# Optimization experiments

Hardware: AMD Instinct MI355X
Metric: run time of the kernel (lower is better)

## Reference

```python
import jax, jax.numpy as jnp
import numpy as np

N = 50000   # nodes
E = 800000  # edges (avg degree 16)
F = 256     # in_feats
H = 4       # num_heads
D = 64      # out_feats per head (H*D == F)


def setup_inputs() -> dict:
    key = jax.random.key(0)
    ks = jax.random.split(key, 10)
    s = 0.02
    HD = H * D
    return {
        "feat": jax.random.normal(ks[0], (N, F), jnp.float32),
        "src": jax.random.randint(ks[1], (E,), 0, N),
        "dst": jax.random.randint(ks[2], (E,), 0, N),
        "Wq": jax.random.normal(ks[3], (HD, F), jnp.float32) * s,
        "bq": jnp.zeros((HD,), jnp.float32),
        "Wk": jax.random.normal(ks[4], (HD, F), jnp.float32) * s,
        "bk": jnp.zeros((HD,), jnp.float32),
        "Wv": jax.random.normal(ks[5], (HD, F), jnp.float32) * s,
        "bv": jnp.zeros((HD,), jnp.float32),
        "Wskip": jax.random.normal(ks[6], (HD, F), jnp.float32) * s,
        "bskip": jnp.zeros((HD,), jnp.float32),
        "Wgate": jax.random.normal(ks[7], (1, 3 * HD), jnp.float32) * s,
        "bgate": jnp.zeros((1,), jnp.float32),
        "ln_w": jnp.ones((HD,), jnp.float32),
        "ln_b": jnp.zeros((HD,), jnp.float32),
        "prelu_a": jnp.float32(0.25),
    }


def reference(feat, src, dst, Wq, bq, Wk, bk, Wv, bv, Wskip, bskip,
              Wgate, bgate, ln_w, ln_b, prelu_a):
    n = feat.shape[0]
    scale = 1.0 / np.sqrt(D).astype(np.float32)
    # projections: note DGL code names q from src nodes, k from dst nodes
    q = (feat @ Wq.T + bq).reshape(n, H, D)
    k = (feat @ Wk.T + bk).reshape(n, H, D)
    v = (feat @ Wv.T + bv).reshape(n, H, D)
    # per-edge scores: u_dot_v('ft','ft') = q[src] . k[dst], scaled
    e = jnp.einsum('ehd,ehd->eh', q[src], k[dst]) * scale  # [E, H]
    # edge softmax over incoming edges of each destination node
    m = jax.ops.segment_max(e, dst, num_segments=n)          # [N, H]
    ex = jnp.exp(e - m[dst])
    denom = jax.ops.segment_sum(ex, dst, num_segments=n)    # [N, H]
    sa = ex / denom[dst]                                     # [E, H]
    # weighted scatter-aggregate: sum_e sa * v[src]
    agg = jax.ops.segment_sum(sa[:, :, None] * v[src], dst, num_segments=n)
    rst = agg.reshape(n, H * D)
    # gated skip connection
    skip = feat @ Wskip.T + bskip
    g = jax.nn.sigmoid(
        jnp.concatenate([skip, rst, skip - rst], axis=-1) @ Wgate.T + bgate)
    rst = g * skip + (1.0 - g) * rst
    # layer norm
    mu = rst.mean(-1, keepdims=True)
    var = rst.var(-1, keepdims=True)
    rst = (rst - mu) * jax.lax.rsqrt(var + 1e-5) * ln_w + ln_b
    # PReLU
    return jnp.where(rst >= 0, rst, prelu_a * rst)
```

## Files before the change

kernel.cpp:

```cpp
#include <hip/hip_runtime.h>
#include <math.h>


typedef __attribute__((ext_vector_type(8))) short short8;
typedef __attribute__((ext_vector_type(4))) float floatx4;
typedef __attribute__((ext_vector_type(2))) float floatx2;
typedef __attribute__((address_space(3))) void lds_void;
typedef __attribute__((address_space(1))) const void gbl_void;

__device__ inline unsigned short f2bf(float x) {
    unsigned int u = __float_as_uint(x);
    u = (u + 0x7fffu + ((u >> 16) & 1u)) >> 16;
    return (unsigned short)u;
}
__device__ inline float bf2f(unsigned short u) {
    return __uint_as_float(((unsigned int)u) << 16);
}

__global__ void prep_kernel(const float* __restrict__ f, ushort* __restrict__ fb,
                            int n_elems, int total_pad,
                            const float* __restrict__ Wq, const float* __restrict__ Wk,
                            const float* __restrict__ Wv, const float* __restrict__ Wsk,
                            const float* __restrict__ bq, const float* __restrict__ bk,
                            const float* __restrict__ bv, const float* __restrict__ bsk,
                            ushort* __restrict__ Wcat, float* __restrict__ bcat,
                            int* __restrict__ counts, int* __restrict__ cursor, int n)
{
    int g = blockIdx.x * blockDim.x + threadIdx.x;
    int featQ = total_pad >> 2;
    if (g < featQ) {
        int i = g * 4;
        float4 v = (i < n_elems) ? *(const float4*)(f + i) : make_float4(0.f, 0.f, 0.f, 0.f);
        ushort4 u;
        u.x = f2bf(v.x); u.y = f2bf(v.y); u.z = f2bf(v.z); u.w = f2bf(v.w);
        *(ushort4*)(fb + i) = u;
        return;
    }
    int g2 = g - featQ;
    if (g2 < 65536) {
        int i = g2 * 4;
        int mat = i >> 16;
        int rem = i & 65535;
        const float* W = (mat == 0) ? Wq : (mat == 1) ? Wk : (mat == 2) ? Wv : Wsk;
        float4 v = *(const float4*)(W + rem);
        ushort4 u;
        u.x = f2bf(v.x); u.y = f2bf(v.y); u.z = f2bf(v.z); u.w = f2bf(v.w);
        *(ushort4*)(Wcat + i) = u;
        return;
    }
    int g3 = g2 - 65536;
    if (g3 < 256) {
        int o = g3 * 4;
        int mat = o >> 8;
        const float* b = (mat == 0) ? bq : (mat == 1) ? bk : (mat == 2) ? bv : bsk;
        *(float4*)(bcat + o) = *(const float4*)(b + (o & 255));
        return;
    }
    int g4 = g3 - 256;
    if (g4 < n) counts[g4] = 0;
    if (g4 == 0) *cursor = 0;
}


__global__ void count_kernel(const int* __restrict__ dst, int* counts, int e) {
    int i = blockIdx.x * blockDim.x + threadIdx.x;
    if (i < e) atomicAdd(&counts[dst[i]], 1);
}

__global__ void alloc_kernel(const int* __restrict__ counts, int* start, int* cur,
                             int* cursor, int n) {
    int i = blockIdx.x * blockDim.x + threadIdx.x;
    int lane = threadIdx.x & 63;
    int c = (i < n) ? counts[i] : 0;
    int incl = c;
#pragma unroll
    for (int d = 1; d < 64; d <<= 1) {
        int t = __shfl_up(incl, d);
        if (lane >= d) incl += t;
    }
    int waveTot = __shfl(incl, 63);
    int base = 0;
    if (lane == 63) base = atomicAdd(cursor, waveTot);
    base = __shfl(base, 63);
    if (i < n) {
        int s = base + incl - c;
        start[i] = s;
        cur[i] = s;
    }
}

__global__ void fill_kernel(const int* __restrict__ dst, const int* __restrict__ src,
                            int* cur, int* srclist, int e) {
    int i = blockIdx.x * blockDim.x + threadIdx.x;
    if (i < e) {
        int pos = atomicAdd(&cur[dst[i]], 1);
        srclist[pos] = src[i];
    }
}

__global__ __launch_bounds__(512) void mfma_gemm(
    const ushort* __restrict__ featb, const ushort* __restrict__ Wcat,
    const float* __restrict__ bcat,
    unsigned char* __restrict__ q8, ushort* __restrict__ kb,
    unsigned char* __restrict__ v8, ushort* __restrict__ sb, int n)
{
    __shared__ ushort At[128 * 32];
    __shared__ ushort Bt[256 * 32];
    int tid = threadIdx.x;
    int lane = tid & 63;
    int wv = tid >> 6;
    int ysel = blockIdx.x;
    int mBase = blockIdx.y * 128;
    int nBlk = ysel * 256;
    int mQuad = (wv & 1) * 64;
    int nQuad = (wv >> 1) * 64;

    floatx4 zero = {0.f, 0.f, 0.f, 0.f};
    floatx4 acc[4][4];
#pragma unroll
    for (int i = 0; i < 4; ++i)
#pragma unroll
        for (int j = 0; j < 4; ++j) acc[i][j] = zero;

    int rsel = lane & 15;
    int ksel = (lane >> 4) * 8;
    int lrow = lane >> 2;
    int lcol = (lane & 3) * 8;

    for (int k0 = 0; k0 < 256; k0 += 32) {
        {
            int row = 16 * wv + lrow;
            const ushort* gp = featb + (size_t)(mBase + row) * 256 + k0 + lcol;
            __builtin_amdgcn_global_load_lds((gbl_void*)gp, (lds_void*)&At[16 * wv * 32], 16, 0, 0);
        }
#pragma unroll
        for (int r = 0; r < 2; ++r) {
            int row = 32 * wv + 16 * r + lrow;
            const ushort* gp = Wcat + (size_t)(nBlk + row) * 256 + k0 + lcol;
            __builtin_amdgcn_global_load_lds((gbl_void*)gp, (lds_void*)&Bt[(32 * wv + 16 * r) * 32], 16, 0, 0);
        }
        __syncthreads();
        short8 af[4], bf[4];
#pragma unroll
        for (int i = 0; i < 4; ++i)
            af[i] = *(const short8*)&At[(mQuad + 16 * i + rsel) * 32 + ksel];
#pragma unroll
        for (int j = 0; j < 4; ++j)
            bf[j] = *(const short8*)&Bt[(nQuad + 16 * j + rsel) * 32 + ksel];
#pragma unroll
        for (int i = 0; i < 4; ++i)
#pragma unroll
            for (int j = 0; j < 4; ++j)
                acc[i][j] = __builtin_amdgcn_mfma_f32_16x16x32_bf16(bf[j], af[i], acc[i][j], 0, 0, 0);
        __syncthreads();
    }

    int rowq4 = (lane >> 4) * 4;
    float4 bias[4];
#pragma unroll
    for (int nt = 0; nt < 4; ++nt)
        bias[nt] = *(const float4*)(bcat + nBlk + nQuad + 16 * nt + rowq4);

    if (ysel == 0 || ysel == 2) {
        unsigned char* outp = (ysel == 0) ? q8 : v8;
#pragma unroll
        for (int mt = 0; mt < 4; ++mt) {
            int m = mBase + mQuad + 16 * mt + (lane & 15);
            if (m < n) {
                unsigned char* rowp = outp + (size_t)m * 256 + nQuad + rowq4;
#pragma unroll
                for (int nt = 0; nt < 4; ++nt) {
                    int pk = __builtin_amdgcn_cvt_pk_fp8_f32(
                        acc[mt][nt][0] + bias[nt].x, acc[mt][nt][1] + bias[nt].y, 0, false);
                    pk = __builtin_amdgcn_cvt_pk_fp8_f32(
                        acc[mt][nt][2] + bias[nt].z, acc[mt][nt][3] + bias[nt].w, pk, true);
                    *(int*)(rowp + 16 * nt) = pk;
                }
            }
        }
    } else {
        ushort* outp = (ysel == 1) ? kb : sb;
#pragma unroll
        for (int mt = 0; mt < 4; ++mt) {
            int m = mBase + mQuad + 16 * mt + (lane & 15);
            if (m < n) {
                ushort* rowp = outp + (size_t)m * 256 + nQuad + rowq4;
#pragma unroll
                for (int nt = 0; nt < 4; ++nt) {
                    uint lo = (uint)f2bf(acc[mt][nt][0] + bias[nt].x)
                            | ((uint)f2bf(acc[mt][nt][1] + bias[nt].y) << 16);
                    uint hi = (uint)f2bf(acc[mt][nt][2] + bias[nt].z)
                            | ((uint)f2bf(acc[mt][nt][3] + bias[nt].w) << 16);
                    *(uint2*)(rowp + 16 * nt) = make_uint2(lo, hi);
                }
            }
        }
    }
}

__global__ __launch_bounds__(256) void node_kernel(
    const unsigned char* __restrict__ q8, const ushort* __restrict__ kb,
    const unsigned char* __restrict__ v8, const ushort* __restrict__ sbuf,
    const int* __restrict__ srclist, const int* __restrict__ start,
    const int* __restrict__ counts,
    const float* __restrict__ Wg, const float* __restrict__ bg,
    const float* __restrict__ lnw, const float* __restrict__ lnb,
    const float* __restrict__ pa,
    float* __restrict__ out, int n, int E)
{
    int wvi = threadIdx.x >> 6;
    int lane = threadIdx.x & 63;
    int node = blockIdx.x * 4 + wvi;
    if (node >= n) return;

    int l32 = lane & 31;
    int half = lane >> 5;
    int f0 = l32 * 8;

    short8 kv = *(const short8*)(kb + (size_t)node * 256 + f0);
    float kf[8];
#pragma unroll
    for (int i = 0; i < 8; ++i) kf[i] = bf2f((unsigned short)kv[i]);

    float acc[8];
#pragma unroll
    for (int i = 0; i < 8; ++i) acc[i] = 0.f;
    float denom = 0.f;

    int sidx = start[node], cnt = counts[node];

    for (int base = 0; base < cnt; base += 64) {
        int m = min(64, cnt - base);
        int batch = srclist[min(sidx + base + lane, E - 1)];
        for (int j = 0; j < m; j += 4) {
            int j0 = j + half;
            int j1 = j0 + 2;
            bool vld0 = j0 < m;
            bool vld1 = j1 < m;
            int s0 = __shfl(batch, vld0 ? j0 : j);
            int s1 = __shfl(batch, vld1 ? j1 : j);
            uint2 qw0 = *(const uint2*)(q8 + (size_t)s0 * 256 + f0);
            uint2 vw0 = *(const uint2*)(v8 + (size_t)s0 * 256 + f0);
            uint2 qw1 = *(const uint2*)(q8 + (size_t)s1 * 256 + f0);
            uint2 vw1 = *(const uint2*)(v8 + (size_t)s1 * 256 + f0);

            floatx2 qa0 = __builtin_amdgcn_cvt_pk_f32_fp8(qw0.x, false);
            floatx2 qa1 = __builtin_amdgcn_cvt_pk_f32_fp8(qw0.x, true);
            floatx2 qa2 = __builtin_amdgcn_cvt_pk_f32_fp8(qw0.y, false);
            floatx2 qa3 = __builtin_amdgcn_cvt_pk_f32_fp8(qw0.y, true);
            floatx2 qb0 = __builtin_amdgcn_cvt_pk_f32_fp8(qw1.x, false);
            floatx2 qb1 = __builtin_amdgcn_cvt_pk_f32_fp8(qw1.x, true);
            floatx2 qb2 = __builtin_amdgcn_cvt_pk_f32_fp8(qw1.y, false);
            floatx2 qb3 = __builtin_amdgcn_cvt_pk_f32_fp8(qw1.y, true);

            float p0 = qa0[0]*kf[0] + qa0[1]*kf[1] + qa1[0]*kf[2] + qa1[1]*kf[3]
                     + qa2[0]*kf[4] + qa2[1]*kf[5] + qa3[0]*kf[6] + qa3[1]*kf[7];
            float p1 = qb0[0]*kf[0] + qb0[1]*kf[1] + qb1[0]*kf[2] + qb1[1]*kf[3]
                     + qb2[0]*kf[4] + qb2[1]*kf[5] + qb3[0]*kf[6] + qb3[1]*kf[7];
            p0 += __shfl_xor(p0, 1);  p1 += __shfl_xor(p1, 1);
            p0 += __shfl_xor(p0, 2);  p1 += __shfl_xor(p1, 2);
            p0 += __shfl_xor(p0, 4);  p1 += __shfl_xor(p1, 4);
            float w0 = vld0 ? __expf(p0 * 0.125f) : 0.f;
            float w1 = vld1 ? __expf(p1 * 0.125f) : 0.f;

            floatx2 va0 = __builtin_amdgcn_cvt_pk_f32_fp8(vw0.x, false);
            floatx2 va1 = __builtin_amdgcn_cvt_pk_f32_fp8(vw0.x, true);
            floatx2 va2 = __builtin_amdgcn_cvt_pk_f32_fp8(vw0.y, false);
            floatx2 va3 = __builtin_amdgcn_cvt_pk_f32_fp8(vw0.y, true);
            floatx2 vb0 = __builtin_amdgcn_cvt_pk_f32_fp8(vw1.x, false);
            floatx2 vb1 = __builtin_amdgcn_cvt_pk_f32_fp8(vw1.x, true);
            floatx2 vb2 = __builtin_amdgcn_cvt_pk_f32_fp8(vw1.y, false);
            floatx2 vb3 = __builtin_amdgcn_cvt_pk_f32_fp8(vw1.y, true);

            denom += w0 + w1;
            acc[0] = fmaf(w0, va0[0], fmaf(w1, vb0[0], acc[0]));
            acc[1] = fmaf(w0, va0[1], fmaf(w1, vb0[1], acc[1]));
            acc[2] = fmaf(w0, va1[0], fmaf(w1, vb1[0], acc[2]));
            acc[3] = fmaf(w0, va1[1], fmaf(w1, vb1[1], acc[3]));
            acc[4] = fmaf(w0, va2[0], fmaf(w1, vb2[0], acc[4]));
            acc[5] = fmaf(w0, va2[1], fmaf(w1, vb2[1], acc[5]));
            acc[6] = fmaf(w0, va3[0], fmaf(w1, vb3[0], acc[6]));
            acc[7] = fmaf(w0, va3[1], fmaf(w1, vb3[1], acc[7]));
        }
    }

#pragma unroll
    for (int i = 0; i < 8; ++i) acc[i] += __shfl_xor(acc[i], 32);
    denom += __shfl_xor(denom, 32);
    float inv = (denom > 0.f) ? 1.f / denom : 0.f;
    float r[8];
#pragma unroll
    for (int i = 0; i < 8; ++i) r[i] = acc[i] * inv;

    short8 sv = *(const short8*)(sbuf + (size_t)node * 256 + f0);
    float s[8];
#pragma unroll
    for (int i = 0; i < 8; ++i) s[i] = bf2f((unsigned short)sv[i]);

    float4 wa0 = *(const float4*)(Wg + f0);
    float4 wa1 = *(const float4*)(Wg + f0 + 4);
    float4 wb0 = *(const float4*)(Wg + 256 + f0);
    float4 wb1 = *(const float4*)(Wg + 256 + f0 + 4);
    float4 wc0 = *(const float4*)(Wg + 512 + f0);
    float4 wc1 = *(const float4*)(Wg + 512 + f0 + 4);
    float z = wa0.x*s[0] + wa0.y*s[1] + wa0.z*s[2] + wa0.w*s[3]
            + wa1.x*s[4] + wa1.y*s[5] + wa1.z*s[6] + wa1.w*s[7]
            + wb0.x*r[0] + wb0.y*r[1] + wb0.z*r[2] + wb0.w*r[3]
            + wb1.x*r[4] + wb1.y*r[5] + wb1.z*r[6] + wb1.w*r[7]
            + wc0.x*(s[0]-r[0]) + wc0.y*(s[1]-r[1]) + wc0.z*(s[2]-r[2]) + wc0.w*(s[3]-r[3])
            + wc1.x*(s[4]-r[4]) + wc1.y*(s[5]-r[5]) + wc1.z*(s[6]-r[6]) + wc1.w*(s[7]-r[7]);
#pragma unroll
    for (int d = 16; d >= 1; d >>= 1) z += __shfl_xor(z, d);
    z += bg[0];
    float g = 1.f / (1.f + __expf(-z));

    float y[8];
#pragma unroll
    for (int i = 0; i < 8; ++i) y[i] = g * s[i] + (1.f - g) * r[i];

    float sum = y[0]+y[1]+y[2]+y[3]+y[4]+y[5]+y[6]+y[7];
#pragma unroll
    for (int d = 16; d >= 1; d >>= 1) sum += __shfl_xor(sum, d);
    float mu = sum * (1.f / 256.f);
    float dv[8];
    float sq = 0.f;
#pragma unroll
    for (int i = 0; i < 8; ++i) { dv[i] = y[i] - mu; sq = fmaf(dv[i], dv[i], sq); }
#pragma unroll
    for (int d = 16; d >= 1; d >>= 1) sq += __shfl_xor(sq, d);
    float rstd = rsqrtf(sq * (1.f / 256.f) + 1e-5f);

    float4 lw0 = *(const float4*)(lnw + f0);
    float4 lw1 = *(const float4*)(lnw + f0 + 4);
    float4 lb0 = *(const float4*)(lnb + f0);
    float4 lb1 = *(const float4*)(lnb + f0 + 4);
    float lwv[8] = {lw0.x, lw0.y, lw0.z, lw0.w, lw1.x, lw1.y, lw1.z, lw1.w};
    float lbv[8] = {lb0.x, lb0.y, lb0.z, lb0.w, lb1.x, lb1.y, lb1.z, lb1.w};
    float ap = pa[0];
    float o[8];
#pragma unroll
    for (int i = 0; i < 8; ++i) {
        float t = dv[i] * rstd * lwv[i] + lbv[i];
        o[i] = (t >= 0.f) ? t : ap * t;
    }

    float4 stv;
    stv.x = half ? o[4] : o[0];
    stv.y = half ? o[5] : o[1];
    stv.z = half ? o[6] : o[2];
    stv.w = half ? o[7] : o[3];
    *(float4*)(out + (size_t)node * 256 + f0 + 4 * half) = stv;
}


extern "C" void kernel_launch(void* const* d_in, const int* in_sizes, int n_in,
                              void* d_out, int out_size, void* d_ws, size_t ws_size,
                              hipStream_t stream)
{
    const float* feat = (const float*)d_in[0];
    const int* src    = (const int*)d_in[1];
    const int* dst    = (const int*)d_in[2];
    const float* Wq   = (const float*)d_in[3];
    const float* bq   = (const float*)d_in[4];
    const float* Wk   = (const float*)d_in[5];
    const float* bk   = (const float*)d_in[6];
    const float* Wv   = (const float*)d_in[7];
    const float* bv   = (const float*)d_in[8];
    const float* Wsk  = (const float*)d_in[9];
    const float* bsk  = (const float*)d_in[10];
    const float* Wg   = (const float*)d_in[11];
    const float* bg   = (const float*)d_in[12];
    const float* lnw  = (const float*)d_in[13];
    const float* lnb  = (const float*)d_in[14];
    const float* pa   = (const float*)d_in[15];

    int N = in_sizes[0] / 256;
    int E = in_sizes[1];
    float* out = (float*)d_out;

    int Mtiles = (N + 127) / 128;
    int Npad = Mtiles * 128;

    char* ws = (char*)d_ws;
    size_t off = 0;
    auto alloc = [&](size_t bytes) { char* p = ws + off; off = (off + bytes + 255) & ~(size_t)255; return p; };
    ushort* featb      = (ushort*)alloc((size_t)Npad * 256 * 2);
    ushort* Wcat       = (ushort*)alloc(1024 * 256 * 2);
    float*  bcat       = (float*) alloc(1024 * 4);
    unsigned char* q8  = (unsigned char*)alloc((size_t)N * 256);
    unsigned char* v8  = (unsigned char*)alloc((size_t)N * 256);
    ushort* kb         = (ushort*)alloc((size_t)N * 256 * 2);
    ushort* sb         = (ushort*)alloc((size_t)N * 256 * 2);
    int* counts        = (int*)alloc((size_t)N * 4);
    int* startv        = (int*)alloc((size_t)N * 4);
    int* cur           = (int*)alloc((size_t)N * 4);
    int* cursor        = (int*)alloc(4);
    int* srclist       = (int*)alloc((size_t)E * 4);

    int totPad = Npad * 256;
    int prepThreads = totPad / 4 + 65536 + 256 + N;
    prep_kernel<<<(prepThreads + 255) / 256, 256, 0, stream>>>(
        feat, featb, N * 256, totPad, Wq, Wk, Wv, Wsk, bq, bk, bv, bsk,
        Wcat, bcat, counts, cursor, N);

    count_kernel<<<(E + 255) / 256, 256, 0, stream>>>(dst, counts, E);
    alloc_kernel<<<(N + 255) / 256, 256, 0, stream>>>(counts, startv, cur, cursor, N);
    fill_kernel<<<(E + 255) / 256, 256, 0, stream>>>(dst, src, cur, srclist, E);

    dim3 gg(4, Mtiles);
    mfma_gemm<<<gg, 512, 0, stream>>>(featb, Wcat, bcat, q8, kb, v8, sb, N);

    node_kernel<<<(N + 3) / 4, 256, 0, stream>>>(q8, kb, v8, sb, srclist, startv, counts,
                                                 Wg, bg, lnw, lnb, pa, out, N, E);
}
```

Before: 350.3 us.

## Widen node-kernel gathers to 16 bytes per lane and fold gate weights

The node kernel now gives each lane 16 features instead of 8, so each wave processes four edges per gather step, each row fetched with 16-byte loads, rather than two edges with 8-byte loads. This halves the number of loop iterations and shortens the per-edge dot-product shuffle reduction. It also precomputes combined gate weights (Wa+Wc and Wb-Wc) in the prep kernel, so the per-node gate dot product reads two vectors instead of three. The cost is more registers per lane (16 accumulators plus 16 key values), which may lower occupancy, and an extra cross-slot reduction at the end.

After: 376.0 us. +7.3%, slower.

```diff
diff --git a/kernel.cpp b/kernel.cpp
--- a/kernel.cpp
+++ b/kernel.cpp
@@ -23,7 +23,9 @@
                             const float* __restrict__ Wv, const float* __restrict__ Wsk,
                             const float* __restrict__ bq, const float* __restrict__ bk,
                             const float* __restrict__ bv, const float* __restrict__ bsk,
+                            const float* __restrict__ Wg,
                             ushort* __restrict__ Wcat, float* __restrict__ bcat,
+                            float* __restrict__ wgs, float* __restrict__ wgr,
                             int* __restrict__ counts, int* __restrict__ cursor, int n)
 {
     int g = blockIdx.x * blockDim.x + threadIdx.x;
@@ -57,8 +59,23 @@
         return;
     }
     int g4 = g3 - 256;
-    if (g4 < n) counts[g4] = 0;
-    if (g4 == 0) *cursor = 0;
+    if (g4 < 64) {
+        int o = g4 * 4;
+        float4 a = *(const float4*)(Wg + o);
+        float4 c = *(const float4*)(Wg + 512 + o);
+        *(float4*)(wgs + o) = make_float4(a.x + c.x, a.y + c.y, a.z + c.z, a.w + c.w);
+        return;
+    }
+    if (g4 < 128) {
+        int o = (g4 - 64) * 4;
+        float4 b = *(const float4*)(Wg + 256 + o);
+        float4 c = *(const float4*)(Wg + 512 + o);
+        *(float4*)(wgr + o) = make_float4(b.x - c.x, b.y - c.y, b.z - c.z, b.w - c.w);
+        return;
+    }
+    int g5 = g4 - 128;
+    if (g5 < n) counts[g5] = 0;
+    if (g5 == 0) *cursor = 0;
 }
 
 
@@ -203,7 +220,8 @@
     const unsigned char* __restrict__ v8, const ushort* __restrict__ sbuf,
     const int* __restrict__ srclist, const int* __restrict__ start,
     const int* __restrict__ counts,
-    const float* __restrict__ Wg, const float* __restrict__ bg,
+    const float* __restrict__ wgs, const float* __restrict__ wgr,
+    const float* __restrict__ bg,
     const float* __restrict__ lnw, const float* __restrict__ lnb,
     const float* __restrict__ pa,
     float* __restrict__ out, int n, int E)
@@ -213,18 +231,24 @@
     int node = blockIdx.x * 4 + wvi;
     if (node >= n) return;
 
-    int l32 = lane & 31;
-    int half = lane >> 5;
-    int f0 = l32 * 8;
-
-    short8 kv = *(const short8*)(kb + (size_t)node * 256 + f0);
-    float kf[8];
-#pragma unroll
-    for (int i = 0; i < 8; ++i) kf[i] = bf2f((unsigned short)kv[i]);
-
-    float acc[8];
-#pragma unroll
-    for (int i = 0; i < 8; ++i) acc[i] = 0.f;
+    int slot = lane >> 4;
+    int sub = lane & 15;
+    int f0 = sub * 16;
+
+    float kf[16];
+    {
+        short8 k0v = *(const short8*)(kb + (size_t)node * 256 + f0);
+        short8 k1v = *(const short8*)(kb + (size_t)node * 256 + f0 + 8);
+#pragma unroll
+        for (int i = 0; i < 8; ++i) {
+            kf[i] = bf2f((unsigned short)k0v[i]);
+            kf[8 + i] = bf2f((unsigned short)k1v[i]);
+        }
+    }
+
+    float acc[16];
+#pragma unroll
+    for (int i = 0; i < 16; ++i) acc[i] = 0.f;
     float denom = 0.f;
 
     int sidx = start[node], cnt = counts[node];
@@ -232,124 +256,186 @@
     for (int base = 0; base < cnt; base += 64) {
         int m = min(64, cnt - base);
         int batch = srclist[min(sidx + base + lane, E - 1)];
-        for (int j = 0; j < m; j += 4) {
-            int j0 = j + half;
-            int j1 = j0 + 2;
-            bool vld0 = j0 < m;
-            bool vld1 = j1 < m;
-            int s0 = __shfl(batch, vld0 ? j0 : j);
-            int s1 = __shfl(batch, vld1 ? j1 : j);
-            uint2 qw0 = *(const uint2*)(q8 + (size_t)s0 * 256 + f0);
-            uint2 vw0 = *(const uint2*)(v8 + (size_t)s0 * 256 + f0);
-            uint2 qw1 = *(const uint2*)(q8 + (size_t)s1 * 256 + f0);
-            uint2 vw1 = *(const uint2*)(v8 + (size_t)s1 * 256 + f0);
-
-            floatx2 qa0 = __builtin_amdgcn_cvt_pk_f32_fp8(qw0.x, false);
-            floatx2 qa1 = __builtin_amdgcn_cvt_pk_f32_fp8(qw0.x, true);
-            floatx2 qa2 = __builtin_amdgcn_cvt_pk_f32_fp8(qw0.y, false);
-            floatx2 qa3 = __builtin_amdgcn_cvt_pk_f32_fp8(qw0.y, true);
-            floatx2 qb0 = __builtin_amdgcn_cvt_pk_f32_fp8(qw1.x, false);
-            floatx2 qb1 = __builtin_amdgcn_cvt_pk_f32_fp8(qw1.x, true);
-            floatx2 qb2 = __builtin_amdgcn_cvt_pk_f32_fp8(qw1.y, false);
-            floatx2 qb3 = __builtin_amdgcn_cvt_pk_f32_fp8(qw1.y, true);
-
-            float p0 = qa0[0]*kf[0] + qa0[1]*kf[1] + qa1[0]*kf[2] + qa1[1]*kf[3]
-                     + qa2[0]*kf[4] + qa2[1]*kf[5] + qa3[0]*kf[6] + qa3[1]*kf[7];
-            float p1 = qb0[0]*kf[0] + qb0[1]*kf[1] + qb1[0]*kf[2] + qb1[1]*kf[3]
-                     + qb2[0]*kf[4] + qb2[1]*kf[5] + qb3[0]*kf[6] + qb3[1]*kf[7];
+        for (int j = 0; j < m; j += 8) {
+            int e0 = j + slot;
+            int e1 = j + 4 + slot;
+            bool vld0 = e0 < m;
+            bool vld1 = e1 < m;
+            int s0 = __shfl(batch, vld0 ? e0 : 0);
+            int s1 = __shfl(batch, vld1 ? e1 : 0);
+            uint4 qw0 = *(const uint4*)(q8 + (size_t)s0 * 256 + f0);
+            uint4 vw0 = *(const uint4*)(v8 + (size_t)s0 * 256 + f0);
+            uint4 qw1 = *(const uint4*)(q8 + (size_t)s1 * 256 + f0);
+            uint4 vw1 = *(const uint4*)(v8 + (size_t)s1 * 256 + f0);
+
+            floatx2 a0 = __builtin_amdgcn_cvt_pk_f32_fp8(qw0.x, false);
+            floatx2 a1 = __builtin_amdgcn_cvt_pk_f32_fp8(qw0.x, true);
+            floatx2 a2 = __builtin_amdgcn_cvt_pk_f32_fp8(qw0.y, false);
+            floatx2 a3 = __builtin_amdgcn_cvt_pk_f32_fp8(qw0.y, true);
+            floatx2 a4 = __builtin_amdgcn_cvt_pk_f32_fp8(qw0.z, false);
+            floatx2 a5 = __builtin_amdgcn_cvt_pk_f32_fp8(qw0.z, true);
+            floatx2 a6 = __builtin_amdgcn_cvt_pk_f32_fp8(qw0.w, false);
+            floatx2 a7 = __builtin_amdgcn_cvt_pk_f32_fp8(qw0.w, true);
+            float c0 = a0[0]*kf[0];  c0 = fmaf(a0[1], kf[1], c0);
+            c0 = fmaf(a1[0], kf[2], c0);  c0 = fmaf(a1[1], kf[3], c0);
+            float c1 = a2[0]*kf[4];  c1 = fmaf(a2[1], kf[5], c1);
+            c1 = fmaf(a3[0], kf[6], c1);  c1 = fmaf(a3[1], kf[7], c1);
+            float c2 = a4[0]*kf[8];  c2 = fmaf(a4[1], kf[9], c2);
+            c2 = fmaf(a5[0], kf[10], c2); c2 = fmaf(a5[1], kf[11], c2);
+            float c3 = a6[0]*kf[12]; c3 = fmaf(a6[1], kf[13], c3);
+            c3 = fmaf(a7[0], kf[14], c3); c3 = fmaf(a7[1], kf[15], c3);
+            float p0 = (c0 + c1) + (c2 + c3);
+
+            floatx2 b0 = __builtin_amdgcn_cvt_pk_f32_fp8(qw1.x, false);
+            floatx2 b1 = __builtin_amdgcn_cvt_pk_f32_fp8(qw1.x, true);
+            floatx2 b2 = __builtin_amdgcn_cvt_pk_f32_fp8(qw1.y, false);
+            floatx2 b3 = __builtin_amdgcn_cvt_pk_f32_fp8(qw1.y, true);
+            floatx2 b4 = __builtin_amdgcn_cvt_pk_f32_fp8(qw1.z, false);
+            floatx2 b5 = __builtin_amdgcn_cvt_pk_f32_fp8(qw1.z, true);
+            floatx2 b6 = __builtin_amdgcn_cvt_pk_f32_fp8(qw1.w, false);
+            floatx2 b7 = __builtin_amdgcn_cvt_pk_f32_fp8(qw1.w, true);
+            float d0 = b0[0]*kf[0];  d0 = fmaf(b0[1], kf[1], d0);
+            d0 = fmaf(b1[0], kf[2], d0);  d0 = fmaf(b1[1], kf[3], d0);
+            float d1 = b2[0]*kf[4];  d1 = fmaf(b2[1], kf[5], d1);
+            d1 = fmaf(b3[0], kf[6], d1);  d1 = fmaf(b3[1], kf[7], d1);
+            float d2 = b4[0]*kf[8];  d2 = fmaf(b4[1], kf[9], d2);
+            d2 = fmaf(b5[0], kf[10], d2); d2 = fmaf(b5[1], kf[11], d2);
+            float d3 = b6[0]*kf[12]; d3 = fmaf(b6[1], kf[13], d3);
+            d3 = fmaf(b7[0], kf[14], d3); d3 = fmaf(b7[1], kf[15], d3);
+            float p1 = (d0 + d1) + (d2 + d3);
+
             p0 += __shfl_xor(p0, 1);  p1 += __shfl_xor(p1, 1);
             p0 += __shfl_xor(p0, 2);  p1 += __shfl_xor(p1, 2);
-            p0 += __shfl_xor(p0, 4);  p1 += __shfl_xor(p1, 4);
             float w0 = vld0 ? __expf(p0 * 0.125f) : 0.f;
             float w1 = vld1 ? __expf(p1 * 0.125f) : 0.f;
-
-            floatx2 va0 = __builtin_amdgcn_cvt_pk_f32_fp8(vw0.x, false);
-            floatx2 va1 = __builtin_amdgcn_cvt_pk_f32_fp8(vw0.x, true);
-            floatx2 va2 = __builtin_amdgcn_cvt_pk_f32_fp8(vw0.y, false);
-            floatx2 va3 = __builtin_amdgcn_cvt_pk_f32_fp8(vw0.y, true);
-            floatx2 vb0 = __builtin_amdgcn_cvt_pk_f32_fp8(vw1.x, false);
-            floatx2 vb1 = __builtin_amdgcn_cvt_pk_f32_fp8(vw1.x, true);
-            floatx2 vb2 = __builtin_amdgcn_cvt_pk_f32_fp8(vw1.y, false);
-            floatx2 vb3 = __builtin_amdgcn_cvt_pk_f32_fp8(vw1.y, true);
-
             denom += w0 + w1;
-            acc[0] = fmaf(w0, va0[0], fmaf(w1, vb0[0], acc[0]));
-            acc[1] = fmaf(w0, va0[1], fmaf(w1, vb0[1], acc[1]));
-            acc[2] = fmaf(w0, va1[0], fmaf(w1, vb1[0], acc[2]));
-            acc[3] = fmaf(w0, va1[1], fmaf(w1, vb1[1], acc[3]));
-            acc[4] = fmaf(w0, va2[0], fmaf(w1, vb2[0], acc[4]));
-            acc[5] = fmaf(w0, va2[1], fmaf(w1, vb2[1], acc[5]));
-            acc[6] = fmaf(w0, va3[0], fmaf(w1, vb3[0], acc[6]));
-            acc[7] = fmaf(w0, va3[1], fmaf(w1, vb3[1], acc[7]));
-        }
-    }
-
-#pragma unroll
-    for (int i = 0; i < 8; ++i) acc[i] += __shfl_xor(acc[i], 32);
+
+            floatx2 x0 = __builtin_amdgcn_cvt_pk_f32_fp8(vw0.x, false);
+            floatx2 x1 = __builtin_amdgcn_cvt_pk_f32_fp8(vw0.x, true);
+            floatx2 x2 = __builtin_amdgcn_cvt_pk_f32_fp8(vw0.y, false);
+            floatx2 x3 = __builtin_amdgcn_cvt_pk_f32_fp8(vw0.y, true);
+            floatx2 x4 = __builtin_amdgcn_cvt_pk_f32_fp8(vw0.z, false);
+            floatx2 x5 = __builtin_amdgcn_cvt_pk_f32_fp8(vw0.z, true);
+            floatx2 x6 = __builtin_amdgcn_cvt_pk_f32_fp8(vw0.w, false);
+            floatx2 x7 = __builtin_amdgcn_cvt_pk_f32_fp8(vw0.w, true);
+            floatx2 y0 = __builtin_amdgcn_cvt_pk_f32_fp8(vw1.x, false);
+            floatx2 y1 = __builtin_amdgcn_cvt_pk_f32_fp8(vw1.x, true);
+            floatx2 y2 = __builtin_amdgcn_cvt_pk_f32_fp8(vw1.y, false);
+            floatx2 y3 = __builtin_amdgcn_cvt_pk_f32_fp8(vw1.y, true);
+            floatx2 y4 = __builtin_amdgcn_cvt_pk_f32_fp8(vw1.z, false);
+            floatx2 y5 = __builtin_amdgcn_cvt_pk_f32_fp8(vw1.z, true);
+            floatx2 y6 = __builtin_amdgcn_cvt_pk_f32_fp8(vw1.w, false);
+            floatx2 y7 = __builtin_amdgcn_cvt_pk_f32_fp8(vw1.w, true);
+            acc[0]  = fmaf(w0, x0[0], fmaf(w1, y0[0], acc[0]));
+            acc[1]  = fmaf(w0, x0[1], fmaf(w1, y0[1], acc[1]));
+            acc[2]  = fmaf(w0, x1[0], fmaf(w1, y1[0], acc[2]));
+            acc[3]  = fmaf(w0, x1[1], fmaf(w1, y1[1], acc[3]));
+            acc[4]  = fmaf(w0, x2[0], fmaf(w1, y2[0], acc[4]));
+            acc[5]  = fmaf(w0, x2[1], fmaf(w1, y2[1], acc[5]));
+            acc[6]  = fmaf(w0, x3[0], fmaf(w1, y3[0], acc[6]));
+            acc[7]  = fmaf(w0, x3[1], fmaf(w1, y3[1], acc[7]));
+            acc[8]  = fmaf(w0, x4[0], fmaf(w1, y4[0], acc[8]));
+            acc[9]  = fmaf(w0, x4[1], fmaf(w1, y4[1], acc[9]));
+            acc[10] = fmaf(w0, x5[0], fmaf(w1, y5[0], acc[10]));
+            acc[11] = fmaf(w0, x5[1], fmaf(w1, y5[1], acc[11]));
+            acc[12] = fmaf(w0, x6[0], fmaf(w1, y6[0], acc[12]));
+            acc[13] = fmaf(w0, x6[1], fmaf(w1, y6[1], acc[13]));
+            acc[14] = fmaf(w0, x7[0], fmaf(w1, y7[0], acc[14]));
+            acc[15] = fmaf(w0, x7[1], fmaf(w1, y7[1], acc[15]));
+        }
+    }
+
+#pragma unroll
+    for (int i = 0; i < 16; ++i) {
+        acc[i] += __shfl_xor(acc[i], 16);
+        acc[i] += __shfl_xor(acc[i], 32);
+    }
+    denom += __shfl_xor(denom, 16);
     denom += __shfl_xor(denom, 32);
     float inv = (denom > 0.f) ? 1.f / denom : 0.f;
-    float r[8];
-#pragma unroll
-    for (int i = 0; i < 8; ++i) r[i] = acc[i] * inv;
-
-    short8 sv = *(const short8*)(sbuf + (size_t)node * 256 + f0);
-    float s[8];
-#pragma unroll
-    for (int i = 0; i < 8; ++i) s[i] = bf2f((unsigned short)sv[i]);
-
-    float4 wa0 = *(const float4*)(Wg + f0);
-    float4 wa1 = *(const float4*)(Wg + f0 + 4);
-    float4 wb0 = *(const float4*)(Wg + 256 + f0);
-    float4 wb1 = *(const float4*)(Wg + 256 + f0 + 4);
-    float4 wc0 = *(const float4*)(Wg + 512 + f0);
-    float4 wc1 = *(const float4*)(Wg + 512 + f0 + 4);
-    float z = wa0.x*s[0] + wa0.y*s[1] + wa0.z*s[2] + wa0.w*s[3]
-            + wa1.x*s[4] + wa1.y*s[5] + wa1.z*s[6] + wa1.w*s[7]
-            + wb0.x*r[0] + wb0.y*r[1] + wb0.z*r[2] + wb0.w*r[3]
-            + wb1.x*r[4] + wb1.y*r[5] + wb1.z*r[6] + wb1.w*r[7]
-            + wc0.x*(s[0]-r[0]) + wc0.y*(s[1]-r[1]) + wc0.z*(s[2]-r[2]) + wc0.w*(s[3]-r[3])
-            + wc1.x*(s[4]-r[4]) + wc1.y*(s[5]-r[5]) + wc1.z*(s[6]-r[6]) + wc1.w*(s[7]-r[7]);
-#pragma unroll
-    for (int d = 16; d >= 1; d >>= 1) z += __shfl_xor(z, d);
+    float r[16];
+#pragma unroll
+    for (int i = 0; i < 16; ++i) r[i] = acc[i] * inv;
+
+    float s[16];
+    {
+        short8 s0v = *(const short8*)(sbuf + (size_t)node * 256 + f0);
+        short8 s1v = *(const short8*)(sbuf + (size_t)node * 256 + f0 + 8);
+#pragma unroll
+        for (int i = 0; i < 8; ++i) {
+            s[i] = bf2f((unsigned short)s0v[i]);
+            s[8 + i] = bf2f((unsigned short)s1v[i]);
+        }
+    }
+
+    float z = 0.f;
+    {
+        float4 g0 = *(const float4*)(wgs + f0);
+        float4 g1 = *(const float4*)(wgs + f0 + 4);
+        float4 g2 = *(const float4*)(wgs + f0 + 8);
+        float4 g3 = *(const float4*)(wgs + f0 + 12);
+        float4 h0 = *(const float4*)(wgr + f0);
+        float4 h1 = *(const float4*)(wgr + f0 + 4);
+        float4 h2 = *(const float4*)(wgr + f0 + 8);
+        float4 h3 = *(const float4*)(wgr + f0 + 12);
+        z = g0.x*s[0] + g0.y*s[1] + g0.z*s[2] + g0.w*s[3]
+          + g1.x*s[4] + g1.y*s[5] + g1.z*s[6] + g1.w*s[7]
+          + g2.x*s[8] + g2.y*s[9] + g2.z*s[10] + g2.w*s[11]
+          + g3.x*s[12] + g3.y*s[13] + g3.z*s[14] + g3.w*s[15]
+          + h0.x*r[0] + h0.y*r[1] + h0.z*r[2] + h0.w*r[3]
+          + h1.x*r[4] + h1.y*r[5] + h1.z*r[6] + h1.w*r[7]
+          + h2.x*r[8] + h2.y*r[9] + h2.z*r[10] + h2.w*r[11]
+          + h3.x*r[12] + h3.y*r[13] + h3.z*r[14] + h3.w*r[15];
+    }
+#pragma unroll
+    for (int d = 8; d >= 1; d >>= 1) z += __shfl_xor(z, d);
     z += bg[0];
     float g = 1.f / (1.f + __expf(-z));
 
-    float y[8];
-#pragma unroll
-    for (int i = 0; i < 8; ++i) y[i] = g * s[i] + (1.f - g) * r[i];
-
-    float sum = y[0]+y[1]+y[2]+y[3]+y[4]+y[5]+y[6]+y[7];
-#pragma unroll
-    for (int d = 16; d >= 1; d >>= 1) sum += __shfl_xor(sum, d);
+    float y[16];
+#pragma unroll
+    for (int i = 0; i < 16; ++i) y[i] = g * s[i] + (1.f - g) * r[i];
+
+    float sum = 0.f;
+#pragma unroll
+    for (int i = 0; i < 16; ++i) sum += y[i];
+#pragma unroll
+    for (int d = 8; d >= 1; d >>= 1) sum += __shfl_xor(sum, d);
     float mu = sum * (1.f / 256.f);
-    float dv[8];
+    float dv[16];
     float sq = 0.f;
 #pragma unroll
-    for (int i = 0; i < 8; ++i) { dv[i] = y[i] - mu; sq = fmaf(dv[i], dv[i], sq); }
-#pragma unroll
-    for (int d = 16; d >= 1; d >>= 1) sq += __shfl_xor(sq, d);
+    for (int i = 0; i < 16; ++i) { dv[i] = y[i] - mu; sq = fmaf(dv[i], dv[i], sq); }
+#pragma unroll
+    for (int d = 8; d >= 1; d >>= 1) sq += __shfl_xor(sq, d);
     float rstd = rsqrtf(sq * (1.f / 256.f) + 1e-5f);
 
-    float4 lw0 = *(const float4*)(lnw + f0);
-    float4 lw1 = *(const float4*)(lnw + f0 + 4);
-    float4 lb0 = *(const float4*)(lnb + f0);
-    float4 lb1 = *(const float4*)(lnb + f0 + 4);
-    float lwv[8] = {lw0.x, lw0.y, lw0.z, lw0.w, lw1.x, lw1.y, lw1.z, lw1.w};
-    float lbv[8] = {lb0.x, lb0.y, lb0.z, lb0.w, lb1.x, lb1.y, lb1.z, lb1.w};
-    float ap = pa[0];
-    float o[8];
-#pragma unroll
-    for (int i = 0; i < 8; ++i) {
-        float t = dv[i] * rstd * lwv[i] + lbv[i];
-        o[i] = (t >= 0.f) ? t : ap * t;
-    }
-
-    float4 stv;
-    stv.x = half ? o[4] : o[0];
-    stv.y = half ? o[5] : o[1];
-    stv.z = half ? o[6] : o[2];
-    stv.w = half ? o[7] : o[3];
-    *(float4*)(out + (size_t)node * 256 + f0 + 4 * half) = stv;
+    float o[16];
+    {
+        float4 lw0 = *(const float4*)(lnw + f0);
+        float4 lw1 = *(const float4*)(lnw + f0 + 4);
+        float4 lw2 = *(const float4*)(lnw + f0 + 8);
+        float4 lw3 = *(const float4*)(lnw + f0 + 12);
+        float4 lb0 = *(const float4*)(lnb + f0);
+        float4 lb1 = *(const float4*)(lnb + f0 + 4);
+        float4 lb2 = *(const float4*)(lnb + f0 + 8);
+        float4 lb3 = *(const float4*)(lnb + f0 + 12);
+        float lwv[16] = {lw0.x, lw0.y, lw0.z, lw0.w, lw1.x, lw1.y, lw1.z, lw1.w,
+                         lw2.x, lw2.y, lw2.z, lw2.w, lw3.x, lw3.y, lw3.z, lw3.w};
+        float lbv[16] = {lb0.x, lb0.y, lb0.z, lb0.w, lb1.x, lb1.y, lb1.z, lb1.w,
+                         lb2.x, lb2.y, lb2.z, lb2.w, lb3.x, lb3.y, lb3.z, lb3.w};
+        float ap = pa[0];
+#pragma unroll
+        for (int i = 0; i < 16; ++i) {
+            float t = dv[i] * rstd * lwv[i] + lbv[i];
+            o[i] = (t >= 0.f) ? t : ap * t;
+        }
+    }
+
+#define SEL(k) ((slot == 0) ? o[k] : (slot == 1) ? o[(k) + 4] : (slot == 2) ? o[(k) + 8] : o[(k) + 12])
+    float4 st = make_float4(SEL(0), SEL(1), SEL(2), SEL(3));
+#undef SEL
+    *(float4*)(out + (size_t)node * 256 + f0 + slot * 4) = st;
 }
 
 
@@ -387,6 +473,8 @@
     ushort* featb      = (ushort*)alloc((size_t)Npad * 256 * 2);
     ushort* Wcat       = (ushort*)alloc(1024 * 256 * 2);
     float*  bcat       = (float*) alloc(1024 * 4);
+    float*  wgs        = (float*) alloc(256 * 4);
+    float*  wgr        = (float*) alloc(256 * 4);
     unsigned char* q8  = (unsigned char*)alloc((size_t)N * 256);
     unsigned char* v8  = (unsigned char*)alloc((size_t)N * 256);
     ushort* kb         = (ushort*)alloc((size_t)N * 256 * 2);
@@ -398,10 +486,10 @@
     int* srclist       = (int*)alloc((size_t)E * 4);
 
     int totPad = Npad * 256;
-    int prepThreads = totPad / 4 + 65536 + 256 + N;
+    int prepThreads = totPad / 4 + 65536 + 256 + 128 + N;
     prep_kernel<<<(prepThreads + 255) / 256, 256, 0, stream>>>(
-        feat, featb, N * 256, totPad, Wq, Wk, Wv, Wsk, bq, bk, bv, bsk,
-        Wcat, bcat, counts, cursor, N);
+        feat, featb, N * 256, totPad, Wq, Wk, Wv, Wsk, bq, bk, bv, bsk, Wg,
+        Wcat, bcat, wgs, wgr, counts, cursor, N);
 
     count_kernel<<<(E + 255) / 256, 256, 0, stream>>>(dst, counts, E);
     alloc_kernel<<<(N + 255) / 256, 256, 0, stream>>>(counts, startv, cur, cursor, N);
@@ -411,5 +499,5 @@
     mfma_gemm<<<gg, 512, 0, stream>>>(featb, Wcat, bcat, q8, kb, v8, sb, N);
 
     node_kernel<<<(N + 3) / 4, 256, 0, stream>>>(q8, kb, v8, sb, srclist, startv, counts,
-                                                 Wg, bg, lnw, lnb, pa, out, N, E);
-}
+                                                 wgs, wgr, bg, lnw, lnb, pa, out, N, E);
+}
```

## Interleave q/v fp8 rows, unroll edge loop to four edges, pre-fold gate weights

Applied to the files above, without the earlier changes.

Stores the fp8 q and v projections interleaved in one 512-byte row per node, so each gathered source node's q and v share a contiguous region. The per-node edge loop now handles four edges per half-wave per iteration instead of two, which puts more gathers in flight. The gate weights are folded once in prep (Ws+Wc, Wr-Wc), so the gate dot product needs fewer loads and FMAs. The cost is higher register pressure in the node kernel and more masked wasted work for nodes with low degree.

New measurement: 353.5 us. No clear change (+0.9%).

```diff
diff --git a/kernel.cpp b/kernel.cpp
--- a/kernel.cpp
+++ b/kernel.cpp
@@ -23,7 +23,9 @@
                             const float* __restrict__ Wv, const float* __restrict__ Wsk,
                             const float* __restrict__ bq, const float* __restrict__ bk,
                             const float* __restrict__ bv, const float* __restrict__ bsk,
+                            const float* __restrict__ Wg,
                             ushort* __restrict__ Wcat, float* __restrict__ bcat,
+                            float* __restrict__ wgs, float* __restrict__ wgr,
                             int* __restrict__ counts, int* __restrict__ cursor, int n)
 {
     int g = blockIdx.x * blockDim.x + threadIdx.x;
@@ -57,8 +59,23 @@
         return;
     }
     int g4 = g3 - 256;
-    if (g4 < n) counts[g4] = 0;
-    if (g4 == 0) *cursor = 0;
+    if (g4 < 64) {
+        int o = g4 * 4;
+        float4 a = *(const float4*)(Wg + o);
+        float4 c = *(const float4*)(Wg + 512 + o);
+        *(float4*)(wgs + o) = make_float4(a.x + c.x, a.y + c.y, a.z + c.z, a.w + c.w);
+        return;
+    }
+    if (g4 < 128) {
+        int o = (g4 - 64) * 4;
+        float4 b = *(const float4*)(Wg + 256 + o);
+        float4 c = *(const float4*)(Wg + 512 + o);
+        *(float4*)(wgr + o) = make_float4(b.x - c.x, b.y - c.y, b.z - c.z, b.w - c.w);
+        return;
+    }
+    int g5 = g4 - 128;
+    if (g5 < n) counts[g5] = 0;
+    if (g5 == 0) *cursor = 0;
 }
 
 
@@ -101,8 +118,8 @@
 __global__ __launch_bounds__(512) void mfma_gemm(
     const ushort* __restrict__ featb, const ushort* __restrict__ Wcat,
     const float* __restrict__ bcat,
-    unsigned char* __restrict__ q8, ushort* __restrict__ kb,
-    unsigned char* __restrict__ v8, ushort* __restrict__ sb, int n)
+    unsigned char* __restrict__ qv8, ushort* __restrict__ kb,
+    ushort* __restrict__ sb, int n)
 {
     __shared__ ushort At[128 * 32];
     __shared__ ushort Bt[256 * 32];
@@ -162,12 +179,12 @@
         bias[nt] = *(const float4*)(bcat + nBlk + nQuad + 16 * nt + rowq4);
 
     if (ysel == 0 || ysel == 2) {
-        unsigned char* outp = (ysel == 0) ? q8 : v8;
+        unsigned char* outp = qv8 + ((ysel == 0) ? 0 : 256);
 #pragma unroll
         for (int mt = 0; mt < 4; ++mt) {
             int m = mBase + mQuad + 16 * mt + (lane & 15);
             if (m < n) {
-                unsigned char* rowp = outp + (size_t)m * 256 + nQuad + rowq4;
+                unsigned char* rowp = outp + (size_t)m * 512 + nQuad + rowq4;
 #pragma unroll
                 for (int nt = 0; nt < 4; ++nt) {
                     int pk = __builtin_amdgcn_cvt_pk_fp8_f32(
@@ -199,11 +216,12 @@
 }
 
 __global__ __launch_bounds__(256) void node_kernel(
-    const unsigned char* __restrict__ q8, const ushort* __restrict__ kb,
-    const unsigned char* __restrict__ v8, const ushort* __restrict__ sbuf,
+    const unsigned char* __restrict__ qv8, const ushort* __restrict__ kb,
+    const ushort* __restrict__ sbuf,
     const int* __restrict__ srclist, const int* __restrict__ start,
     const int* __restrict__ counts,
-    const float* __restrict__ Wg, const float* __restrict__ bg,
+    const float* __restrict__ wgs, const float* __restrict__ wgr,
+    const float* __restrict__ bg,
     const float* __restrict__ lnw, const float* __restrict__ lnb,
     const float* __restrict__ pa,
     float* __restrict__ out, int n, int E)
@@ -232,55 +250,103 @@
     for (int base = 0; base < cnt; base += 64) {
         int m = min(64, cnt - base);
         int batch = srclist[min(sidx + base + lane, E - 1)];
-        for (int j = 0; j < m; j += 4) {
-            int j0 = j + half;
-            int j1 = j0 + 2;
-            bool vld0 = j0 < m;
-            bool vld1 = j1 < m;
-            int s0 = __shfl(batch, vld0 ? j0 : j);
-            int s1 = __shfl(batch, vld1 ? j1 : j);
-            uint2 qw0 = *(const uint2*)(q8 + (size_t)s0 * 256 + f0);
-            uint2 vw0 = *(const uint2*)(v8 + (size_t)s0 * 256 + f0);
-            uint2 qw1 = *(const uint2*)(q8 + (size_t)s1 * 256 + f0);
-            uint2 vw1 = *(const uint2*)(v8 + (size_t)s1 * 256 + f0);
-
-            floatx2 qa0 = __builtin_amdgcn_cvt_pk_f32_fp8(qw0.x, false);
-            floatx2 qa1 = __builtin_amdgcn_cvt_pk_f32_fp8(qw0.x, true);
-            floatx2 qa2 = __builtin_amdgcn_cvt_pk_f32_fp8(qw0.y, false);
-            floatx2 qa3 = __builtin_amdgcn_cvt_pk_f32_fp8(qw0.y, true);
-            floatx2 qb0 = __builtin_amdgcn_cvt_pk_f32_fp8(qw1.x, false);
-            floatx2 qb1 = __builtin_amdgcn_cvt_pk_f32_fp8(qw1.x, true);
-            floatx2 qb2 = __builtin_amdgcn_cvt_pk_f32_fp8(qw1.y, false);
-            floatx2 qb3 = __builtin_amdgcn_cvt_pk_f32_fp8(qw1.y, true);
-
-            float p0 = qa0[0]*kf[0] + qa0[1]*kf[1] + qa1[0]*kf[2] + qa1[1]*kf[3]
-                     + qa2[0]*kf[4] + qa2[1]*kf[5] + qa3[0]*kf[6] + qa3[1]*kf[7];
-            float p1 = qb0[0]*kf[0] + qb0[1]*kf[1] + qb1[0]*kf[2] + qb1[1]*kf[3]
-                     + qb2[0]*kf[4] + qb2[1]*kf[5] + qb3[0]*kf[6] + qb3[1]*kf[7];
-            p0 += __shfl_xor(p0, 1);  p1 += __shfl_xor(p1, 1);
-            p0 += __shfl_xor(p0, 2);  p1 += __shfl_xor(p1, 2);
-            p0 += __shfl_xor(p0, 4);  p1 += __shfl_xor(p1, 4);
-            float w0 = vld0 ? __expf(p0 * 0.125f) : 0.f;
-            float w1 = vld1 ? __expf(p1 * 0.125f) : 0.f;
-
-            floatx2 va0 = __builtin_amdgcn_cvt_pk_f32_fp8(vw0.x, false);
-            floatx2 va1 = __builtin_amdgcn_cvt_pk_f32_fp8(vw0.x, true);
-            floatx2 va2 = __builtin_amdgcn_cvt_pk_f32_fp8(vw0.y, false);
-            floatx2 va3 = __builtin_amdgcn_cvt_pk_f32_fp8(vw0.y, true);
-            floatx2 vb0 = __builtin_amdgcn_cvt_pk_f32_fp8(vw1.x, false);
-            floatx2 vb1 = __builtin_amdgcn_cvt_pk_f32_fp8(vw1.x, true);
-            floatx2 vb2 = __builtin_amdgcn_cvt_pk_f32_fp8(vw1.y, false);
-            floatx2 vb3 = __builtin_amdgcn_cvt_pk_f32_fp8(vw1.y, true);
-
-            denom += w0 + w1;
-            acc[0] = fmaf(w0, va0[0], fmaf(w1, vb0[0], acc[0]));
-            acc[1] = fmaf(w0, va0[1], fmaf(w1, vb0[1], acc[1]));
-            acc[2] = fmaf(w0, va1[0], fmaf(w1, vb1[0], acc[2]));
-            acc[3] = fmaf(w0, va1[1], fmaf(w1, vb1[1], acc[3]));
-            acc[4] = fmaf(w0, va2[0], fmaf(w1, vb2[0], acc[4]));
-            acc[5] = fmaf(w0, va2[1], fmaf(w1, vb2[1], acc[5]));
-            acc[6] = fmaf(w0, va3[0], fmaf(w1, vb3[0], acc[6]));
-            acc[7] = fmaf(w0, va3[1], fmaf(w1, vb3[1], acc[7]));
+        for (int j = 0; j < m; j += 8) {
+            int e0 = j + half;
+            int e1 = e0 + 2;
+            int e2 = e0 + 4;
+            int e3 = e0 + 6;
+            bool vld0 = e0 < m;
+            bool vld1 = e1 < m;
+            bool vld2 = e2 < m;
+            bool vld3 = e3 < m;
+            int s0 = __shfl(batch, vld0 ? e0 : 0);
+            int s1 = __shfl(batch, vld1 ? e1 : 0);
+            int s2 = __shfl(batch, vld2 ? e2 : 0);
+            int s3 = __shfl(batch, vld3 ? e3 : 0);
+            const unsigned char* p0 = qv8 + (size_t)s0 * 512 + f0;
+            const unsigned char* p1 = qv8 + (size_t)s1 * 512 + f0;
+            const unsigned char* p2 = qv8 + (size_t)s2 * 512 + f0;
+            const unsigned char* p3 = qv8 + (size_t)s3 * 512 + f0;
+            uint2 qw0 = *(const uint2*)p0;
+            uint2 qw1 = *(const uint2*)p1;
+            uint2 qw2 = *(const uint2*)p2;
+            uint2 qw3 = *(const uint2*)p3;
+            uint2 vw0 = *(const uint2*)(p0 + 256);
+            uint2 vw1 = *(const uint2*)(p1 + 256);
+            uint2 vw2 = *(const uint2*)(p2 + 256);
+            uint2 vw3 = *(const uint2*)(p3 + 256);
+
+            floatx2 a0l = __builtin_amdgcn_cvt_pk_f32_fp8(qw0.x, false);
+            floatx2 a0h = __builtin_amdgcn_cvt_pk_f32_fp8(qw0.x, true);
+            floatx2 a0m = __builtin_amdgcn_cvt_pk_f32_fp8(qw0.y, false);
+            floatx2 a0t = __builtin_amdgcn_cvt_pk_f32_fp8(qw0.y, true);
+            floatx2 a1l = __builtin_amdgcn_cvt_pk_f32_fp8(qw1.x, false);
+            floatx2 a1h = __builtin_amdgcn_cvt_pk_f32_fp8(qw1.x, true);
+            floatx2 a1m = __builtin_amdgcn_cvt_pk_f32_fp8(qw1.y, false);
+            floatx2 a1t = __builtin_amdgcn_cvt_pk_f32_fp8(qw1.y, true);
+            floatx2 a2l = __builtin_amdgcn_cvt_pk_f32_fp8(qw2.x, false);
+            floatx2 a2h = __builtin_amdgcn_cvt_pk_f32_fp8(qw2.x, true);
+            floatx2 a2m = __builtin_amdgcn_cvt_pk_f32_fp8(qw2.y, false);
+            floatx2 a2t = __builtin_amdgcn_cvt_pk_f32_fp8(qw2.y, true);
+            floatx2 a3l = __builtin_amdgcn_cvt_pk_f32_fp8(qw3.x, false);
+            floatx2 a3h = __builtin_amdgcn_cvt_pk_f32_fp8(qw3.x, true);
+            floatx2 a3m = __builtin_amdgcn_cvt_pk_f32_fp8(qw3.y, false);
+            floatx2 a3t = __builtin_amdgcn_cvt_pk_f32_fp8(qw3.y, true);
+
+            float p0f = a0l[0]*kf[0]; p0f = fmaf(a0l[1], kf[1], p0f);
+            p0f = fmaf(a0h[0], kf[2], p0f); p0f = fmaf(a0h[1], kf[3], p0f);
+            p0f = fmaf(a0m[0], kf[4], p0f); p0f = fmaf(a0m[1], kf[5], p0f);
+            p0f = fmaf(a0t[0], kf[6], p0f); p0f = fmaf(a0t[1], kf[7], p0f);
+            float p1f = a1l[0]*kf[0]; p1f = fmaf(a1l[1], kf[1], p1f);
+            p1f = fmaf(a1h[0], kf[2], p1f); p1f = fmaf(a1h[1], kf[3], p1f);
+            p1f = fmaf(a1m[0], kf[4], p1f); p1f = fmaf(a1m[1], kf[5], p1f);
+            p1f = fmaf(a1t[0], kf[6], p1f); p1f = fmaf(a1t[1], kf[7], p1f);
+            float p2f = a2l[0]*kf[0]; p2f = fmaf(a2l[1], kf[1], p2f);
+            p2f = fmaf(a2h[0], kf[2], p2f); p2f = fmaf(a2h[1], kf[3], p2f);
+            p2f = fmaf(a2m[0], kf[4], p2f); p2f = fmaf(a2m[1], kf[5], p2f);
+            p2f = fmaf(a2t[0], kf[6], p2f); p2f = fmaf(a2t[1], kf[7], p2f);
+            float p3f = a3l[0]*kf[0]; p3f = fmaf(a3l[1], kf[1], p3f);
+            p3f = fmaf(a3h[0], kf[2], p3f); p3f = fmaf(a3h[1], kf[3], p3f);
+            p3f = fmaf(a3m[0], kf[4], p3f); p3f = fmaf(a3m[1], kf[5], p3f);
+            p3f = fmaf(a3t[0], kf[6], p3f); p3f = fmaf(a3t[1], kf[7], p3f);
+
+            p0f += __shfl_xor(p0f, 1);  p1f += __shfl_xor(p1f, 1);
+            p2f += __shfl_xor(p2f, 1);  p3f += __shfl_xor(p3f, 1);
+            p0f += __shfl_xor(p0f, 2);  p1f += __shfl_xor(p1f, 2);
+            p2f += __shfl_xor(p2f, 2);  p3f += __shfl_xor(p3f, 2);
+            p0f += __shfl_xor(p0f, 4);  p1f += __shfl_xor(p1f, 4);
+            p2f += __shfl_xor(p2f, 4);  p3f += __shfl_xor(p3f, 4);
+            float w0 = vld0 ? __expf(p0f * 0.125f) : 0.f;
+            float w1 = vld1 ? __expf(p1f * 0.125f) : 0.f;
+            float w2 = vld2 ? __expf(p2f * 0.125f) : 0.f;
+            float w3 = vld3 ? __expf(p3f * 0.125f) : 0.f;
+            denom += (w0 + w1) + (w2 + w3);
+
+            floatx2 x0l = __builtin_amdgcn_cvt_pk_f32_fp8(vw0.x, false);
+            floatx2 x0h = __builtin_amdgcn_cvt_pk_f32_fp8(vw0.x, true);
+            floatx2 x0m = __builtin_amdgcn_cvt_pk_f32_fp8(vw0.y, false);
+            floatx2 x0t = __builtin_amdgcn_cvt_pk_f32_fp8(vw0.y, true);
+            floatx2 x1l = __builtin_amdgcn_cvt_pk_f32_fp8(vw1.x, false);
+            floatx2 x1h = __builtin_amdgcn_cvt_pk_f32_fp8(vw1.x, true);
+            floatx2 x1m = __builtin_amdgcn_cvt_pk_f32_fp8(vw1.y, false);
+            floatx2 x1t = __builtin_amdgcn_cvt_pk_f32_fp8(vw1.y, true);
+            floatx2 x2l = __builtin_amdgcn_cvt_pk_f32_fp8(vw2.x, false);
+            floatx2 x2h = __builtin_amdgcn_cvt_pk_f32_fp8(vw2.x, true);
+            floatx2 x2m = __builtin_amdgcn_cvt_pk_f32_fp8(vw2.y, false);
+            floatx2 x2t = __builtin_amdgcn_cvt_pk_f32_fp8(vw2.y, true);
+            floatx2 x3l = __builtin_amdgcn_cvt_pk_f32_fp8(vw3.x, false);
+            floatx2 x3h = __builtin_amdgcn_cvt_pk_f32_fp8(vw3.x, true);
+            floatx2 x3m = __builtin_amdgcn_cvt_pk_f32_fp8(vw3.y, false);
+            floatx2 x3t = __builtin_amdgcn_cvt_pk_f32_fp8(vw3.y, true);
+
+            acc[0] = fmaf(w0, x0l[0], fmaf(w1, x1l[0], fmaf(w2, x2l[0], fmaf(w3, x3l[0], acc[0]))));
+            acc[1] = fmaf(w0, x0l[1], fmaf(w1, x1l[1], fmaf(w2, x2l[1], fmaf(w3, x3l[1], acc[1]))));
+            acc[2] = fmaf(w0, x0h[0], fmaf(w1, x1h[0], fmaf(w2, x2h[0], fmaf(w3, x3h[0], acc[2]))));
+            acc[3] = fmaf(w0, x0h[1], fmaf(w1, x1h[1], fmaf(w2, x2h[1], fmaf(w3, x3h[1], acc[3]))));
+            acc[4] = fmaf(w0, x0m[0], fmaf(w1, x1m[0], fmaf(w2, x2m[0], fmaf(w3, x3m[0], acc[4]))));
+            acc[5] = fmaf(w0, x0m[1], fmaf(w1, x1m[1], fmaf(w2, x2m[1], fmaf(w3, x3m[1], acc[5]))));
+            acc[6] = fmaf(w0, x0t[0], fmaf(w1, x1t[0], fmaf(w2, x2t[0], fmaf(w3, x3t[0], acc[6]))));
+            acc[7] = fmaf(w0, x0t[1], fmaf(w1, x1t[1], fmaf(w2, x2t[1], fmaf(w3, x3t[1], acc[7]))));
         }
     }
 
@@ -297,18 +363,14 @@
 #pragma unroll
     for (int i = 0; i < 8; ++i) s[i] = bf2f((unsigned short)sv[i]);
 
-    float4 wa0 = *(const float4*)(Wg + f0);
-    float4 wa1 = *(const float4*)(Wg + f0 + 4);
-    float4 wb0 = *(const float4*)(Wg + 256 + f0);
-    float4 wb1 = *(const float4*)(Wg + 256 + f0 + 4);
-    float4 wc0 = *(const float4*)(Wg + 512 + f0);
-    float4 wc1 = *(const float4*)(Wg + 512 + f0 + 4);
-    float z = wa0.x*s[0] + wa0.y*s[1] + wa0.z*s[2] + wa0.w*s[3]
-            + wa1.x*s[4] + wa1.y*s[5] + wa1.z*s[6] + wa1.w*s[7]
-            + wb0.x*r[0] + wb0.y*r[1] + wb0.z*r[2] + wb0.w*r[3]
-            + wb1.x*r[4] + wb1.y*r[5] + wb1.z*r[6] + wb1.w*r[7]
-            + wc0.x*(s[0]-r[0]) + wc0.y*(s[1]-r[1]) + wc0.z*(s[2]-r[2]) + wc0.w*(s[3]-r[3])
-            + wc1.x*(s[4]-r[4]) + wc1.y*(s[5]-r[5]) + wc1.z*(s[6]-r[6]) + wc1.w*(s[7]-r[7]);
+    float4 g0 = *(const float4*)(wgs + f0);
+    float4 g1 = *(const float4*)(wgs + f0 + 4);
+    float4 h0 = *(const float4*)(wgr + f0);
+    float4 h1 = *(const float4*)(wgr + f0 + 4);
+    float z = g0.x*s[0] + g0.y*s[1] + g0.z*s[2] + g0.w*s[3]
+            + g1.x*s[4] + g1.y*s[5] + g1.z*s[6] + g1.w*s[7]
+            + h0.x*r[0] + h0.y*r[1] + h0.z*r[2] + h0.w*r[3]
+            + h1.x*r[4] + h1.y*r[5] + h1.z*r[6] + h1.w*r[7];
 #pragma unroll
     for (int d = 16; d >= 1; d >>= 1) z += __shfl_xor(z, d);
     z += bg[0];
@@ -387,8 +449,9 @@
     ushort* featb      = (ushort*)alloc((size_t)Npad * 256 * 2);
     ushort* Wcat       = (ushort*)alloc(1024 * 256 * 2);
     float*  bcat       = (float*) alloc(1024 * 4);
-    unsigned char* q8  = (unsigned char*)alloc((size_t)N * 256);
-    unsigned char* v8  = (unsigned char*)alloc((size_t)N * 256);
+    float*  wgs        = (float*) alloc(256 * 4);
+    float*  wgr        = (float*) alloc(256 * 4);
+    unsigned char* qv8 = (unsigned char*)alloc((size_t)N * 512);
     ushort* kb         = (ushort*)alloc((size_t)N * 256 * 2);
     ushort* sb         = (ushort*)alloc((size_t)N * 256 * 2);
     int* counts        = (int*)alloc((size_t)N * 4);
@@ -398,18 +461,18 @@
     int* srclist       = (int*)alloc((size_t)E * 4);
 
     int totPad = Npad * 256;
-    int prepThreads = totPad / 4 + 65536 + 256 + N;
+    int prepThreads = totPad / 4 + 65536 + 256 + 128 + N;
     prep_kernel<<<(prepThreads + 255) / 256, 256, 0, stream>>>(
-        feat, featb, N * 256, totPad, Wq, Wk, Wv, Wsk, bq, bk, bv, bsk,
-        Wcat, bcat, counts, cursor, N);
+        feat, featb, N * 256, totPad, Wq, Wk, Wv, Wsk, bq, bk, bv, bsk, Wg,
+        Wcat, bcat, wgs, wgr, counts, cursor, N);
 
     count_kernel<<<(E + 255) / 256, 256, 0, stream>>>(dst, counts, E);
     alloc_kernel<<<(N + 255) / 256, 256, 0, stream>>>(counts, startv, cur, cursor, N);
     fill_kernel<<<(E + 255) / 256, 256, 0, stream>>>(dst, src, cur, srclist, E);
 
     dim3 gg(4, Mtiles);
-    mfma_gemm<<<gg, 512, 0, stream>>>(featb, Wcat, bcat, q8, kb, v8, sb, N);
-
-    node_kernel<<<(N + 3) / 4, 256, 0, stream>>>(q8, kb, v8, sb, srclist, startv, counts,
-                                                 Wg, bg, lnw, lnb, pa, out, N, E);
-}
+    mfma_gemm<<<gg, 512, 0, stream>>>(featb, Wcat, bcat, qv8, kb, sb, N);
+
+    node_kernel<<<(N + 3) / 4, 256, 0, stream>>>(qv8, kb, sb, srclist, startv, counts,
+                                                 wgs, wgr, bg, lnw, lnb, pa, out, N, E);
+}
```
